# Performance work log

Measured on AMD Instinct MI355X. Metric: run time of the kernel, lower is better.

Reference implementation:

```python
import math
import jax, jax.numpy as jnp
import numpy as np

B, N, NC = 2, 2048, 256
C_S, C_COND, C_Z, C_H, H, PQK, PV = 384, 256, 128, 16, 12, 4, 8
BQ, BK = 32, 128
NBLK = N // BQ
INF, EPS = 1e5, 1e-8
CONCAT = C_Z // 4 + C_H + PV * 4  # per-head output feature dim


def _ln(x, w=None, b=None, eps=1e-5):
    mu = jnp.mean(x, -1, keepdims=True)
    var = jnp.mean((x - mu) ** 2, -1, keepdims=True)
    y = (x - mu) * jax.lax.rsqrt(var + eps)
    if w is not None:
        y = y * w
    if b is not None:
        y = y + b
    return y


def _quat_to_rot(q):
    w, x, y, z = q[..., 0], q[..., 1], q[..., 2], q[..., 3]
    r = jnp.stack([
        1 - 2 * (y * y + z * z), 2 * (x * y - w * z), 2 * (x * z + w * y),
        2 * (x * y + w * z), 1 - 2 * (x * x + z * z), 2 * (y * z - w * x),
        2 * (x * z - w * y), 2 * (y * z + w * x), 1 - 2 * (x * x + y * y),
    ], axis=-1)
    return r.reshape(q.shape[:-1] + (3, 3))


def setup_inputs() -> dict:
    key = jax.random.key(0)
    ks = jax.random.split(key, 24)
    p = lambda k, shp: 0.02 * jax.random.normal(k, shp, dtype=jnp.float32)
    quat = jax.random.normal(ks[5], (B, N, 4), dtype=jnp.float32)
    quat = quat / jnp.linalg.norm(quat, axis=-1, keepdims=True)
    hc = H * C_H
    return {
        "s": jax.random.normal(ks[0], (B, N, C_S), dtype=jnp.float32),
        "cond": jax.random.normal(ks[1], (B, NC, C_COND), dtype=jnp.float32),
        "z": jax.random.normal(ks[2], (B, NBLK, BQ, BK, C_Z), dtype=jnp.float32),
        "trans": jax.random.normal(ks[3], (B, N, 3), dtype=jnp.float32),
        "rots": _quat_to_rot(quat),
        "s_mask": jnp.ones((B, N), dtype=jnp.float32),
        "cond_to_s_idx": jax.random.randint(ks[4], (B, N), 0, NC),
        "ln_cond_w": jnp.ones((C_COND,), dtype=jnp.float32),
        "lin_cond_W": p(ks[6], (C_S, C_COND)),
        "lin_cond_b": jnp.zeros((C_S,), dtype=jnp.float32),
        "lin_cond_nb_W": p(ks[7], (C_S, C_COND)),
        "ln_z_w": jnp.ones((C_Z,), dtype=jnp.float32),
        "ln_z_b": jnp.zeros((C_Z,), dtype=jnp.float32),
        "Wq": p(ks[8], (hc, C_S)),
        "Wk": p(ks[9], (hc, C_S)),
        "Wv": p(ks[10], (hc, C_S)),
        "Wqp": p(ks[11], (H * PQK * 3, C_S)),
        "Wkvp": p(ks[12], (H * (PQK + PV) * 3, C_S)),
        "Wb": p(ks[13], (H, C_Z)),
        "Wdz": p(ks[14], (C_Z // 4, C_Z)),
        "head_weights": jnp.full((H,), 0.541324854612918, dtype=jnp.float32),
        "Wout": p(ks[15], (C_S, H * CONCAT)),
    }


def _forward(s, cond, z, trans, rots, s_mask, cond_to_s_idx,
             ln_cond_w, lin_cond_W, lin_cond_b, lin_cond_nb_W, ln_z_w, ln_z_b,
             Wq, Wk, Wv, Wqp, Wkvp, Wb, Wdz, head_weights, Wout):
    # ---- GatherAdaLN ----
    s_n = _ln(s)
    c_n = _ln(cond, ln_cond_w)
    idx3 = jnp.broadcast_to(cond_to_s_idx[..., None], (B, N, C_S))
    gate = jnp.take_along_axis(c_n @ lin_cond_W.T + lin_cond_b, idx3, axis=1) * s_mask[..., None]
    bias = jnp.take_along_axis(c_n @ lin_cond_nb_W.T, idx3, axis=1) * s_mask[..., None]
    s2 = s_n * jax.nn.sigmoid(gate) + bias
    # ---- pair LN ----
    zn = _ln(z, ln_z_w, ln_z_b)
    # ---- block gather (to_queries / to_keys) ----
    pad = (BK - BQ) // 2
    base = jnp.arange(NBLK)[:, None] * BQ + jnp.arange(BK)[None, :] - pad  # [NBLK, BK]
    validk = (base >= 0) & (base < N)
    kidx = jnp.clip(base, 0, N - 1)

    def to_q(x):
        return x.reshape((B, NBLK, BQ) + x.shape[2:])

    def to_k(x):
        g = x[:, kidx]  # [B, NBLK, BK, ...]
        vm = validk.reshape((1, NBLK, BK) + (1,) * (g.ndim - 3)).astype(g.dtype)
        return g * vm

    q_in, k_in = to_q(s2), to_k(s2)
    q_t, q_R = to_q(trans), to_q(rots)
    k_t = to_k(trans)
    k_R = jnp.where(validk[None, :, :, None, None], rots[:, kidx], jnp.eye(3, dtype=rots.dtype))
    # ---- scalar q/k/v ----
    q = (q_in @ Wq.T).reshape(B, NBLK, BQ, H, C_H)
    k = (k_in @ Wk.T).reshape(B, NBLK, BK, H, C_H)
    v = (k_in @ Wv.T).reshape(B, NBLK, BK, H, C_H)
    # ---- point q/k/v in global frames ----
    qp = (q_in @ Wqp.T).reshape(B, NBLK, BQ, H * PQK, 3)
    q_pts = (jnp.einsum('bnqij,bnqpj->bnqpi', q_R, qp) + q_t[..., None, :]).reshape(B, NBLK, BQ, H, PQK, 3)
    kvp = (k_in @ Wkvp.T).reshape(B, NBLK, BK, H * (PQK + PV), 3)
    kv_pts = (jnp.einsum('bnkij,bnkpj->bnkpi', k_R, kvp) + k_t[..., None, :]).reshape(B, NBLK, BK, H, PQK + PV, 3)
    k_pts, v_pts = kv_pts[..., :PQK, :], kv_pts[..., PQK:, :]
    # ---- logits ----
    b_bias = zn @ Wb.T  # [B,NBLK,BQ,BK,H]
    a = jnp.einsum('bnqhc,bnkhc->bnqkh', q, k) * math.sqrt(1.0 / (3 * C_H)) + b_bias * math.sqrt(1.0 / 3)
    # point bias (cdist form)
    pt = -2.0 * jnp.einsum('bnqhpd,bnkhpd->bnqkh', q_pts, k_pts)
    pt = pt + jnp.sum(q_pts ** 2, axis=(-1, -2))[..., None, :]
    pt = pt + jnp.sum(k_pts ** 2, axis=(-1, -2))[..., None, :, :]
    hw = jax.nn.softplus(head_weights) * math.sqrt(1.0 / (3 * (PQK * 9.0 / 2)))
    pt = pt * hw * (-0.5)
    qm = to_q(s_mask[..., None])  # [B,NBLK,BQ,1]
    km = to_k(s_mask[..., None])  # [B,NBLK,BK,1]
    amask = INF * (qm * jnp.swapaxes(km, -1, -2) - 1.0)  # [B,NBLK,BQ,BK]
    a = a + pt + amask[..., None]
    a = jax.nn.softmax(jnp.swapaxes(a, -1, -2), axis=-1)  # [B,NBLK,BQ,H,BK]
    # ---- outputs ----
    o = jnp.einsum('bnqhk,bnkhc->bnqhc', a, v).reshape(B, NBLK, BQ, H * C_H)
    o_pt = jnp.einsum('bnqhk,bnkhvc->bnqhvc', a, v_pts)
    o_pt = jnp.einsum('bnqij,bnqhvi->bnqhvj', q_R, o_pt - q_t[..., None, None, :])  # R^T (p - t)
    o_pt_norm = jnp.sqrt(jnp.sum(o_pt ** 2, -1) + EPS).reshape(B, NBLK, BQ, H * PV)
    o_pt_flat = o_pt.reshape(B, NBLK, BQ, H * PV * 3)
    pair_z = zn @ Wdz.T  # [B,NBLK,BQ,BK,C_Z//4]
    o_pair = jnp.einsum('bnqhk,bnqkc->bnqhc', a, pair_z).reshape(B, NBLK, BQ, H * (C_Z // 4))
    feats = jnp.concatenate([o, o_pt_flat, o_pt_norm, o_pair], axis=-1)
    return (feats @ Wout.T).reshape(B, N, C_S)


def reference(s, cond, z, trans, rots, s_mask, cond_to_s_idx,
              ln_cond_w, lin_cond_W, lin_cond_b, lin_cond_nb_W, ln_z_w, ln_z_b,
              Wq, Wk, Wv, Wqp, Wkvp, Wb, Wdz, head_weights, Wout):
    return _forward(s, cond, z, trans, rots, s_mask, cond_to_s_idx,
                    ln_cond_w, lin_cond_W, lin_cond_b, lin_cond_nb_W, ln_z_w, ln_z_b,
                    Wq, Wk, Wv, Wqp, Wkvp, Wb, Wdz, head_weights, Wout)
```

## Files before the change

kernel.cpp:

```cpp
#include <hip/hip_runtime.h>
#include <math.h>

constexpr int Bv = 2, Nv = 2048, NCv = 256;
constexpr int CSv = 384, CCONDv = 256;
constexpr int CHv = 16, Hv = 12, PQKv = 4, PVv = 8;
constexpr int BQv = 32, BKv = 128, NBLKv = 64;
constexpr int HC = Hv * CHv;
constexpr int QPD = Hv * PQKv * 3;
constexpr int FEAT = 960;
constexpr int PROJW = 1152;
constexpr float S1 = 0.14433756729740643f;
constexpr float S2 = 0.5773502691896258f;
constexpr float HWS = 0.13608276348795434f;

typedef __attribute__((ext_vector_type(8))) short bf16x8;
typedef __attribute__((ext_vector_type(4))) float f32x4;

__device__ __forceinline__ short f2bf(float f) {
    unsigned u = __float_as_uint(f);
    u += 0x7FFF + ((u >> 16) & 1);
    return (short)(u >> 16);
}
__device__ __forceinline__ float bf2f(short s) {
    return __uint_as_float(((unsigned)(unsigned short)s) << 16);
}
__device__ __forceinline__ unsigned pk2(short lo, short hi) {
    return ((unsigned)(unsigned short)lo) | (((unsigned)(unsigned short)hi) << 16);
}

union BF8 { short s[8]; bf16x8 v; };

__device__ __forceinline__ float blockReduceSum(float v, volatile float* red, int t, int nthr) {
    #pragma unroll
    for (int off = 32; off > 0; off >>= 1) v += __shfl_down(v, off, 64);
    int wid = t >> 6, lane = t & 63, nw = nthr >> 6;
    __syncthreads();
    if (lane == 0) red[wid] = v;
    __syncthreads();
    float r = 0.f;
    for (int w = 0; w < nw; ++w) r += red[w];
    return r;
}

__global__ __launch_bounds__(256) void k_wcvt(const float* __restrict__ Wq,
                                              const float* __restrict__ Wk,
                                              const float* __restrict__ Wv,
                                              const float* __restrict__ Wqp,
                                              const float* __restrict__ Wkvp,
                                              const float* __restrict__ Wg,
                                              const float* __restrict__ Wnb,
                                              short* __restrict__ wsW,
                                              short* __restrict__ wsW2) {
    int i4 = blockIdx.x * 256 + threadIdx.x;
    int off = i4 * 4;
    const float* src;
    short* dst;
    int rel;
    if (off < 442368) {
        dst = wsW; rel = off;
        if (rel < 73728) src = Wq;
        else if (rel < 147456) { src = Wk; rel -= 73728; }
        else if (rel < 221184) { src = Wv; rel -= 147456; }
        else if (rel < 276480) { src = Wqp; rel -= 221184; }
        else { src = Wkvp; rel -= 276480; }
        float4 v = *(const float4*)(src + rel);
        *(uint2*)(dst + off) = make_uint2(pk2(f2bf(v.x), f2bf(v.y)), pk2(f2bf(v.z), f2bf(v.w)));
    } else if (off < 442368 + 196608) {
        int o2 = off - 442368;
        rel = o2;
        if (rel < 98304) src = Wg; else { src = Wnb; rel -= 98304; }
        float4 v = *(const float4*)(src + rel);
        *(uint2*)(wsW2 + o2) = make_uint2(pk2(f2bf(v.x), f2bf(v.y)), pk2(f2bf(v.z), f2bf(v.w)));
    }
}

__global__ __launch_bounds__(256) void k_gemm_bt(const short* __restrict__ A,
                                                 const short* __restrict__ B,
                                                 float* __restrict__ C,
                                                 int K, int ldc) {
    __shared__ short As[128 * 40];
    __shared__ short Bs[128 * 40];
    int t = threadIdx.x;
    int m0 = blockIdx.x * 128, n0 = blockIdx.y * 128;
    int wv = t >> 6, lane = t & 63, lr = lane & 15, quad = lane >> 4;
    int mq = (wv & 1) * 64, nq = (wv >> 1) * 64;
    f32x4 acc[4][4];
    #pragma unroll
    for (int i = 0; i < 4; ++i)
        #pragma unroll
        for (int j = 0; j < 4; ++j) acc[i][j] = 0;

    int r0 = t >> 2, c8 = (t & 3) * 8;
    int r1 = (t + 256) >> 2, c81 = ((t + 256) & 3) * 8;

    for (int k0 = 0; k0 < K; k0 += 32) {
        uint4 a0 = *(const uint4*)(A + (size_t)(m0 + r0) * K + k0 + c8);
        uint4 a1 = *(const uint4*)(A + (size_t)(m0 + r1) * K + k0 + c81);
        uint4 b0 = *(const uint4*)(B + (size_t)(n0 + r0) * K + k0 + c8);
        uint4 b1 = *(const uint4*)(B + (size_t)(n0 + r1) * K + k0 + c81);
        *(uint4*)&As[r0 * 40 + c8] = a0;
        *(uint4*)&As[r1 * 40 + c81] = a1;
        *(uint4*)&Bs[r0 * 40 + c8] = b0;
        *(uint4*)&Bs[r1 * 40 + c81] = b1;
        __syncthreads();
        bf16x8 af[4], bf[4];
        #pragma unroll
        for (int i = 0; i < 4; ++i) {
            af[i] = *(const bf16x8*)&As[(mq + i * 16 + lr) * 40 + quad * 8];
            bf[i] = *(const bf16x8*)&Bs[(nq + i * 16 + lr) * 40 + quad * 8];
        }
        #pragma unroll
        for (int i = 0; i < 4; ++i)
            #pragma unroll
            for (int j = 0; j < 4; ++j)
                acc[i][j] = __builtin_amdgcn_mfma_f32_16x16x32_bf16(af[i], bf[j], acc[i][j], 0, 0, 0);
        __syncthreads();
    }
    #pragma unroll
    for (int i = 0; i < 4; ++i) {
        #pragma unroll
        for (int j = 0; j < 4; ++j) {
            int col = n0 + nq + j * 16 + lr;
            #pragma unroll
            for (int r = 0; r < 4; ++r) {
                int row = m0 + mq + i * 16 + quad * 4 + r;
                C[(size_t)row * ldc + col] = acc[i][j][r];
            }
        }
    }
}

__global__ __launch_bounds__(256) void k_condln(const float* __restrict__ cond,
                                                const float* __restrict__ lnw,
                                                short* __restrict__ cnbf) {
    __shared__ float red[4];
    int row = blockIdx.x;
    int t = threadIdx.x;
    float c = cond[row * CCONDv + t];
    float mu = blockReduceSum(c, red, t, 256) * (1.f / CCONDv);
    float d = c - mu;
    float var = blockReduceSum(d * d, red, t, 256) * (1.f / CCONDv);
    cnbf[row * CCONDv + t] = f2bf(d * rsqrtf(var + 1e-5f) * lnw[t]);
}

__global__ __launch_bounds__(128) void k_s2(const float* __restrict__ s,
                                            const float* __restrict__ gb,
                                            const float* __restrict__ bg,
                                            const int* __restrict__ cidx,
                                            const float* __restrict__ smask,
                                            short* __restrict__ s2bf) {
    __shared__ float red[4];
    int row = blockIdx.x;
    int t = threadIdx.x;
    const float* sr = s + (size_t)row * CSv;
    float x0 = sr[t], x1 = sr[t + 128], x2 = sr[t + 256];
    float mu = blockReduceSum(x0 + x1 + x2, red, t, 128) * (1.f / CSv);
    float d0 = x0 - mu, d1 = x1 - mu, d2 = x2 - mu;
    float var = blockReduceSum(d0 * d0 + d1 * d1 + d2 * d2, red, t, 128) * (1.f / CSv);
    float rs = rsqrtf(var + 1e-5f);
    int b = row / Nv;
    int ci = cidx[row];
    float m = smask[row];
    const float* gbr = gb + (size_t)(b * NCv + ci) * 768;
    float dd[3] = {d0, d1, d2};
    #pragma unroll
    for (int j = 0; j < 3; ++j) {
        int cc = t + j * 128;
        float sn = dd[j] * rs;
        float g = (gbr[cc] + bg[cc]) * m, bi = gbr[384 + cc] * m;
        s2bf[(size_t)row * CSv + cc] = f2bf(sn * (1.f / (1.f + expf(-g))) + bi);
    }
}

__global__ __launch_bounds__(192) void k_post(const float* __restrict__ proj,
                                              const float* __restrict__ rots,
                                              const float* __restrict__ trans,
                                              float* __restrict__ qpts,
                                              float* __restrict__ kpts,
                                              float* __restrict__ vpts,
                                              float* __restrict__ qsq,
                                              float* __restrict__ ksq) {
    __shared__ float R[9], tr[3];
    int row = blockIdx.x;
    int t = threadIdx.x;
    if (t < 9) R[t] = rots[(size_t)row * 9 + t];
    if (t < 3) tr[t] = trans[(size_t)row * 3 + t];
    __syncthreads();
    const float* pr = proj + (size_t)row * PROJW + 576;
    float x = pr[t * 3 + 0], y = pr[t * 3 + 1], z = pr[t * 3 + 2];
    float ox = R[0] * x + R[1] * y + R[2] * z + tr[0];
    float oy = R[3] * x + R[4] * y + R[5] * z + tr[1];
    float oz = R[6] * x + R[7] * y + R[8] * z + tr[2];
    float sq = ox * ox + oy * oy + oz * oz;
    if (t < 48) {
        qpts[(size_t)row * QPD + t * 3 + 0] = ox;
        qpts[(size_t)row * QPD + t * 3 + 1] = oy;
        qpts[(size_t)row * QPD + t * 3 + 2] = oz;
        float s4 = sq + __shfl_xor(sq, 1, 64);
        s4 += __shfl_xor(s4, 2, 64);
        if ((t & 3) == 0) qsq[(size_t)row * Hv + (t >> 2)] = s4;
    } else {
        int p = t - 48;
        int h = p / 12, pp = p % 12;
        if (pp < PQKv) {
            kpts[(size_t)row * QPD + (h * PQKv + pp) * 3 + 0] = ox;
            kpts[(size_t)row * QPD + (h * PQKv + pp) * 3 + 1] = oy;
            kpts[(size_t)row * QPD + (h * PQKv + pp) * 3 + 2] = oz;
            float s4 = sq + __shfl_xor(sq, 1, 64);
            s4 += __shfl_xor(s4, 2, 64);
            if (pp == 0) ksq[(size_t)row * Hv + h] = s4;
        } else {
            int vi = h * PVv + pp - PQKv;
            vpts[(size_t)row * (Hv * PVv * 3) + vi * 3 + 0] = ox;
            vpts[(size_t)row * (Hv * PVv * 3) + vi * 3 + 1] = oy;
            vpts[(size_t)row * (Hv * PVv * 3) + vi * 3 + 2] = oz;
        }
    }
}

__global__ __launch_bounds__(256) void k_prep(const float* __restrict__ Wb,
                                              const float* __restrict__ Wdz,
                                              const float* __restrict__ lnw,
                                              const float* __restrict__ lnb,
                                              short* __restrict__ wp,
                                              float* __restrict__ SB) {
    int t = threadIdx.x;
    if (t < 176) {
        int c = t >> 2, q = t & 3;
        const float* wrow = (c < 12) ? (Wb + (size_t)c * 128) : (Wdz + (size_t)(c - 12) * 128);
        float sacc = 0.f, bacc = 0.f;
        for (int i = q * 32; i < q * 32 + 32; ++i) {
            float wf = wrow[i] * lnw[i];
            short bs = f2bf(wf);
            wp[c * 128 + i] = bs;
            sacc += bf2f(bs);
            bacc += lnb[i] * wrow[i];
        }
        sacc += __shfl_xor(sacc, 1, 64); sacc += __shfl_xor(sacc, 2, 64);
        bacc += __shfl_xor(bacc, 1, 64); bacc += __shfl_xor(bacc, 2, 64);
        if (q == 0) { SB[c] = sacc; SB[48 + c] = bacc; }
    }
    for (int i = t; i < 512; i += 256) wp[44 * 128 + i] = 0;
    if (t >= 176 && t < 180) { SB[t - 132] = 0.f; SB[48 + t - 132] = 0.f; }
}

__global__ __launch_bounds__(256) void k_zproj2(const float* __restrict__ z,
                                                const short* __restrict__ wp,
                                                const float* __restrict__ SB,
                                                float* __restrict__ bbias2,
                                                short* __restrict__ pairzT) {
    __shared__ short zbuf[128 * 136];
    __shared__ short wbuf[48 * 136];
    __shared__ float muL[128], rsL[128], SL[48], BL[48];
    int t = threadIdx.x;
    int bid = blockIdx.x;
    int bblk = bid >> 5, qq = bid & 31;
    size_t row0 = (size_t)bid * 128;

    for (int idx = t; idx < 768; idx += 256) {
        int c = idx >> 4, k8 = idx & 15;
        uint4 v = *(const uint4*)(wp + c * 128 + k8 * 8);
        *(uint4*)&wbuf[c * 136 + k8 * 8] = v;
    }
    if (t < 96) {
        float v = SB[t];
        if (t < 48) SL[t] = v; else BL[t - 48] = v;
    }

    const float4* zsrc = (const float4*)(z + row0 * 128);
    #pragma unroll
    for (int it = 0; it < 16; ++it) {
        int f = it * 256 + t;
        int r = f >> 5, c4 = f & 31;
        float4 v = zsrc[f];
        short s0 = f2bf(v.x), s1 = f2bf(v.y), s2v = f2bf(v.z), s3 = f2bf(v.w);
        *(uint2*)&zbuf[r * 136 + c4 * 4] = make_uint2(pk2(s0, s1), pk2(s2v, s3));
        float sm = v.x + v.y + v.z + v.w;
        float sq = v.x * v.x + v.y * v.y + v.z * v.z + v.w * v.w;
        #pragma unroll
        for (int off = 1; off <= 16; off <<= 1) {
            sm += __shfl_xor(sm, off, 64);
            sq += __shfl_xor(sq, off, 64);
        }
        if ((t & 31) == 0) {
            float mu = sm * (1.f / 128.f);
            float var = sq * (1.f / 128.f) - mu * mu;
            muL[r] = mu;
            rsL[r] = rsqrtf(var + 1e-5f);
        }
    }
    __syncthreads();

    int wv = t >> 6, lane = t & 63;
    int lr = lane & 15, quad = lane >> 4;
    int mb = wv * 32;
    f32x4 acc[2][3];
    #pragma unroll
    for (int i = 0; i < 2; ++i)
        #pragma unroll
        for (int j = 0; j < 3; ++j) acc[i][j] = 0;
    #pragma unroll
    for (int kt = 0; kt < 4; ++kt) {
        int ko = kt * 32 + quad * 8;
        bf16x8 a0 = *(const bf16x8*)&zbuf[(mb + lr) * 136 + ko];
        bf16x8 a1 = *(const bf16x8*)&zbuf[(mb + 16 + lr) * 136 + ko];
        bf16x8 b0 = *(const bf16x8*)&wbuf[lr * 136 + ko];
        bf16x8 b1 = *(const bf16x8*)&wbuf[(16 + lr) * 136 + ko];
        bf16x8 b2 = *(const bf16x8*)&wbuf[(32 + lr) * 136 + ko];
        acc[0][0] = __builtin_amdgcn_mfma_f32_16x16x32_bf16(a0, b0, acc[0][0], 0, 0, 0);
        acc[0][1] = __builtin_amdgcn_mfma_f32_16x16x32_bf16(a0, b1, acc[0][1], 0, 0, 0);
        acc[0][2] = __builtin_amdgcn_mfma_f32_16x16x32_bf16(a0, b2, acc[0][2], 0, 0, 0);
        acc[1][0] = __builtin_amdgcn_mfma_f32_16x16x32_bf16(a1, b0, acc[1][0], 0, 0, 0);
        acc[1][1] = __builtin_amdgcn_mfma_f32_16x16x32_bf16(a1, b1, acc[1][1], 0, 0, 0);
        acc[1][2] = __builtin_amdgcn_mfma_f32_16x16x32_bf16(a1, b2, acc[1][2], 0, 0, 0);
    }

    float* bb_base = bbias2 + (size_t)(bblk * 12) * 4096 + qq * 128;
    short* pz_base = pairzT + (size_t)bid * 32 * 128;
    #pragma unroll
    for (int mt = 0; mt < 2; ++mt) {
        #pragma unroll
        for (int nt = 0; nt < 3; ++nt) {
            int col = nt * 16 + lr;
            int kbase = mb + mt * 16 + quad * 4;
            float ov[4];
            #pragma unroll
            for (int r4 = 0; r4 < 4; ++r4) {
                int rl = kbase + r4;
                ov[r4] = rsL[rl] * (acc[mt][nt][r4] - muL[rl] * SL[col]) + BL[col];
            }
            if (col < 12) {
                *(float4*)&bb_base[(size_t)col * 4096 + kbase] =
                    make_float4(ov[0], ov[1], ov[2], ov[3]);
            } else if (col < 44) {
                int c = col - 12;
                *(uint2*)&pz_base[c * 128 + kbase] =
                    make_uint2(pk2(f2bf(ov[0]), f2bf(ov[1])), pk2(f2bf(ov[2]), f2bf(ov[3])));
            }
        }
    }
}

__global__ __launch_bounds__(512) void k_attn_main(const float* __restrict__ proj,
                                                   const float* __restrict__ qpts,
                                                   const float* __restrict__ kpts,
                                                   const float* __restrict__ vpts,
                                                   const float* __restrict__ qsq,
                                                   const float* __restrict__ ksq,
                                                   const float* __restrict__ bbias2,
                                                   const float* __restrict__ smask,
                                                   const float* __restrict__ head_w,
                                                   short* __restrict__ Aws,
                                                   float* __restrict__ optraw,
                                                   float* __restrict__ feats) {
    __shared__ short kfrag[128 * 40];
    __shared__ short qfrag[32 * 40];
    __shared__ short vtile[128 * 48];
    __shared__ float sc[32 * 132];
    __shared__ short Abuf[32 * 136];
    __shared__ float rowb[32], qmL[32], colb[128], kmL[128];
    __shared__ int   nkgL[128];

    int t = threadIdx.x;
    int hg = blockIdx.x & 1;
    int bblk = blockIdx.x >> 1;
    int b = bblk >> 6, blk = bblk & 63;
    int wv = t >> 6, lane = t & 63;
    int lr = lane & 15, quad = lane >> 4;

    if (t < 128) {
        int nkrel = blk * BQv + t - 48;
        bool valid = (nkrel >= 0) && (nkrel < Nv);
        int nkg = valid ? (b * Nv + nkrel) : -1;
        nkgL[t] = nkg;
        kmL[t] = valid ? smask[nkg] : 0.f;
    }
    __syncthreads();

    for (int hh = 0; hh < 6; ++hh) {
        int h = hg * 6 + hh;
        float hw = log1pf(expf(head_w[h])) * HWS;

        {
            int k = t >> 2, c4 = (t & 3) << 2;
            int g = nkgL[k];
            float4 v = (g >= 0) ? *(const float4*)&proj[(size_t)g * PROJW + 192 + h * 16 + c4]
                                : make_float4(0, 0, 0, 0);
            *(uint2*)&kfrag[k * 40 + c4] =
                make_uint2(pk2(f2bf(v.x), f2bf(v.y)), pk2(f2bf(v.z), f2bf(v.w)));
            kfrag[k * 40 + 28 + (t & 3)] = 0;
        }
        if (t < 384) {
            int k = t / 3, c4 = (t % 3) * 4;
            int g = nkgL[k];
            float4 v = (g >= 0) ? *(const float4*)&kpts[(size_t)g * QPD + h * 12 + c4]
                                : make_float4(0, 0, 0, 0);
            *(uint2*)&kfrag[k * 40 + 16 + c4] =
                make_uint2(pk2(f2bf(v.x), f2bf(v.y)), pk2(f2bf(v.z), f2bf(v.w)));
        }
        if (t < 128) {
            int g = nkgL[t];
            colb[t] = (g >= 0) ? (-0.5f * hw * ksq[(size_t)g * Hv + h]) : 0.f;
            int q = t >> 2, c4 = (t & 3) << 2;
            int nqg = b * Nv + blk * BQv + q;
            float4 v = *(const float4*)&proj[(size_t)nqg * PROJW + h * 16 + c4];
            *(uint2*)&qfrag[q * 40 + c4] =
                make_uint2(pk2(f2bf(S1 * v.x), f2bf(S1 * v.y)),
                           pk2(f2bf(S1 * v.z), f2bf(S1 * v.w)));
            qfrag[q * 40 + 28 + (t & 3)] = 0;
        }
        if (t < 96) {
            int q = t / 3, c4 = (t % 3) * 4;
            int nqg = b * Nv + blk * BQv + q;
            float4 v = *(const float4*)&qpts[(size_t)nqg * QPD + h * 12 + c4];
            *(uint2*)&qfrag[q * 40 + 16 + c4] =
                make_uint2(pk2(f2bf(hw * v.x), f2bf(hw * v.y)),
                           pk2(f2bf(hw * v.z), f2bf(hw * v.w)));
        }
        if (t < 32) {
            int nqg = b * Nv + blk * BQv + t;
            rowb[t] = -0.5f * hw * qsq[(size_t)nqg * Hv + h];
            qmL[t] = smask[nqg];
        }
        for (int i = t; i < 128 * 48; i += 512) {
            int k = i / 48, c = i % 48;
            int g = nkgL[k];
            float v = 0.f;
            if (g >= 0) {
                if (c < 16) v = proj[(size_t)g * PROJW + 384 + h * 16 + c];
                else if (c < 40) v = vpts[(size_t)g * (Hv * PVv * 3) + h * 24 + (c - 16)];
            }
            vtile[k * 48 + c] = f2bf(v);
        }
        __syncthreads();

        f32x4 d[2];
        d[0] = 0; d[1] = 0;
        {
            bf16x8 bfr = *(const bf16x8*)&kfrag[(wv * 16 + lr) * 40 + quad * 8];
            bf16x8 a0 = *(const bf16x8*)&qfrag[lr * 40 + quad * 8];
            bf16x8 a1 = *(const bf16x8*)&qfrag[(16 + lr) * 40 + quad * 8];
            d[0] = __builtin_amdgcn_mfma_f32_16x16x32_bf16(a0, bfr, d[0], 0, 0, 0);
            d[1] = __builtin_amdgcn_mfma_f32_16x16x32_bf16(a1, bfr, d[1], 0, 0, 0);
        }
        {
            const float* bb = bbias2 + (size_t)(bblk * 12 + h) * 4096;
            #pragma unroll
            for (int mt = 0; mt < 2; ++mt) {
                #pragma unroll
                for (int r = 0; r < 4; ++r) {
                    int q = mt * 16 + quad * 4 + r;
                    int k = wv * 16 + lr;
                    float logit = d[mt][r] + rowb[q] + colb[k]
                                + 1e5f * (qmL[q] * kmL[k] - 1.f)
                                + S2 * bb[q * 128 + k];
                    sc[q * 132 + k] = logit;
                }
            }
        }
        __syncthreads();

        {
            int q = t >> 4, i0 = (t & 15) * 8;
            float v[8];
            float m = -3.0e38f;
            #pragma unroll
            for (int j = 0; j < 8; ++j) { v[j] = sc[q * 132 + i0 + j]; m = fmaxf(m, v[j]); }
            #pragma unroll
            for (int off = 1; off <= 8; off <<= 1) m = fmaxf(m, __shfl_xor(m, off, 64));
            float ssum = 0.f;
            #pragma unroll
            for (int j = 0; j < 8; ++j) { v[j] = expf(v[j] - m); ssum += v[j]; }
            #pragma unroll
            for (int off = 1; off <= 8; off <<= 1) ssum += __shfl_xor(ssum, off, 64);
            float inv = 1.f / ssum;
            short a8[8];
            #pragma unroll
            for (int j = 0; j < 8; ++j) a8[j] = f2bf(v[j] * inv);
            uint4 packed = make_uint4(pk2(a8[0], a8[1]), pk2(a8[2], a8[3]),
                                      pk2(a8[4], a8[5]), pk2(a8[6], a8[7]));
            *(uint4*)&Abuf[q * 136 + i0] = packed;
            *(uint4*)&Aws[((size_t)(bblk * 32 + q) * 12 + h) * 128 + i0] = packed;
        }
        __syncthreads();

        if (wv < 6) {
            int mt = wv & 1, nt = wv >> 1;
            f32x4 acc = 0;
            #pragma unroll
            for (int kt = 0; kt < 4; ++kt) {
                bf16x8 a = *(const bf16x8*)&Abuf[(mt * 16 + lr) * 136 + quad * 8 + kt * 32];
                BF8 bb8;
                #pragma unroll
                for (int j = 0; j < 8; ++j)
                    bb8.s[j] = vtile[(kt * 32 + quad * 8 + j) * 48 + nt * 16 + lr];
                acc = __builtin_amdgcn_mfma_f32_16x16x32_bf16(a, bb8.v, acc, 0, 0, 0);
            }
            int c = nt * 16 + lr;
            #pragma unroll
            for (int r = 0; r < 4; ++r) {
                int q = mt * 16 + quad * 4 + r;
                size_t nqg = (size_t)b * Nv + blk * BQv + q;
                if (c < 16) feats[nqg * FEAT + h * 16 + c] = acc[r];
                else if (c < 40) optraw[nqg * 288 + h * 24 + (c - 16)] = acc[r];
            }
        }
        __syncthreads();
    }
}

__global__ __launch_bounds__(64) void k_pair(const short* __restrict__ Aws,
                                             const short* __restrict__ pairzT,
                                             const float* __restrict__ optraw,
                                             const float* __restrict__ rots,
                                             const float* __restrict__ trans,
                                             float* __restrict__ feats) {
    __shared__ unsigned apad_u[16 * 68];
    __shared__ unsigned ppad_u[32 * 68];
    __shared__ float Rt[12];
    int t = threadIdx.x;
    int bid = blockIdx.x;
    int lr = t & 15, quad = t >> 4;

    if (t < 9) Rt[t] = rots[(size_t)bid * 9 + t];
    if (t < 3) Rt[9 + t] = trans[(size_t)bid * 3 + t];

    const unsigned* Asrc = (const unsigned*)(Aws + (size_t)bid * 12 * 128);
    for (int i = t; i < 768; i += 64) {
        int h = i >> 6, w32 = i & 63;
        apad_u[h * 68 + w32] = Asrc[h * 64 + w32];
    }
    for (int i = t; i < 272; i += 64) apad_u[12 * 68 + i] = 0;
    const unsigned* Psrc = (const unsigned*)(pairzT + (size_t)bid * 32 * 128);
    for (int i = t; i < 2048; i += 64) {
        int c = i >> 6, w32 = i & 63;
        ppad_u[c * 68 + w32] = Psrc[c * 64 + w32];
    }
    __syncthreads();

    const short* apad = (const short*)apad_u;
    const short* ppad = (const short*)ppad_u;
    f32x4 acc0 = 0, acc1 = 0;
    #pragma unroll
    for (int kt = 0; kt < 4; ++kt) {
        int ko = quad * 8 + kt * 32;
        bf16x8 a = *(const bf16x8*)&apad[lr * 136 + ko];
        bf16x8 b0 = *(const bf16x8*)&ppad[lr * 136 + ko];
        bf16x8 b1 = *(const bf16x8*)&ppad[(16 + lr) * 136 + ko];
        acc0 = __builtin_amdgcn_mfma_f32_16x16x32_bf16(a, b0, acc0, 0, 0, 0);
        acc1 = __builtin_amdgcn_mfma_f32_16x16x32_bf16(a, b1, acc1, 0, 0, 0);
    }
    float* frow = feats + (size_t)bid * FEAT;
    #pragma unroll
    for (int r = 0; r < 4; ++r) {
        int hh = quad * 4 + r;
        if (hh < 12) {
            frow[576 + hh * 32 + lr] = acc0[r];
            frow[576 + hh * 32 + 16 + lr] = acc1[r];
        }
    }

    for (int p = t; p < 96; p += 64) {
        float x = optraw[(size_t)bid * 288 + p * 3 + 0] - Rt[9];
        float y = optraw[(size_t)bid * 288 + p * 3 + 1] - Rt[10];
        float z = optraw[(size_t)bid * 288 + p * 3 + 2] - Rt[11];
        float lx = Rt[0] * x + Rt[3] * y + Rt[6] * z;
        float ly = Rt[1] * x + Rt[4] * y + Rt[7] * z;
        float lz = Rt[2] * x + Rt[5] * y + Rt[8] * z;
        frow[192 + p * 3 + 0] = lx;
        frow[192 + p * 3 + 1] = ly;
        frow[192 + p * 3 + 2] = lz;
        frow[480 + p] = sqrtf(lx * lx + ly * ly + lz * lz + 1e-8f);
    }
}

__global__ __launch_bounds__(256) void k_out(const float* __restrict__ A,
                                             const float* __restrict__ Wo,
                                             float* __restrict__ C) {
    __shared__ float As[32][65];
    __shared__ float Bs[32][65];
    int t = threadIdx.x;
    int m0 = blockIdx.x * 64;
    int c0 = blockIdx.y * 64;
    int tx = t & 15, ty = t >> 4;
    int lr = t >> 2, lk = (t & 3) * 8;
    float acc[4][4] = {};
    for (int k0 = 0; k0 < FEAT; k0 += 32) {
        const float4* ap = (const float4*)(A + (size_t)(m0 + lr) * FEAT + k0 + lk);
        const float4* bp = (const float4*)(Wo + (size_t)(c0 + lr) * FEAT + k0 + lk);
        float4 a0 = ap[0], a1 = ap[1];
        float4 b0 = bp[0], b1 = bp[1];
        As[lk + 0][lr] = a0.x; As[lk + 1][lr] = a0.y; As[lk + 2][lr] = a0.z; As[lk + 3][lr] = a0.w;
        As[lk + 4][lr] = a1.x; As[lk + 5][lr] = a1.y; As[lk + 6][lr] = a1.z; As[lk + 7][lr] = a1.w;
        Bs[lk + 0][lr] = b0.x; Bs[lk + 1][lr] = b0.y; Bs[lk + 2][lr] = b0.z; Bs[lk + 3][lr] = b0.w;
        Bs[lk + 4][lr] = b1.x; Bs[lk + 5][lr] = b1.y; Bs[lk + 6][lr] = b1.z; Bs[lk + 7][lr] = b1.w;
        __syncthreads();
        #pragma unroll
        for (int kk = 0; kk < 32; ++kk) {
            float a4[4], b4[4];
            #pragma unroll
            for (int i = 0; i < 4; ++i) a4[i] = As[kk][ty * 4 + i];
            #pragma unroll
            for (int j = 0; j < 4; ++j) b4[j] = Bs[kk][tx * 4 + j];
            #pragma unroll
            for (int i = 0; i < 4; ++i)
                #pragma unroll
                for (int j = 0; j < 4; ++j) acc[i][j] += a4[i] * b4[j];
        }
        __syncthreads();
    }
    #pragma unroll
    for (int i = 0; i < 4; ++i)
        #pragma unroll
        for (int j = 0; j < 4; ++j)
            C[(size_t)(m0 + ty * 4 + i) * CSv + c0 + tx * 4 + j] = acc[i][j];
}

extern "C" void kernel_launch(void* const* d_in, const int* in_sizes, int n_in,
                              void* d_out, int out_size, void* d_ws, size_t ws_size,
                              hipStream_t stream) {
    const float* s          = (const float*)d_in[0];
    const float* cond       = (const float*)d_in[1];
    const float* z          = (const float*)d_in[2];
    const float* trans      = (const float*)d_in[3];
    const float* rots       = (const float*)d_in[4];
    const float* smask      = (const float*)d_in[5];
    const int*   cidx       = (const int*)d_in[6];
    const float* ln_cond_w  = (const float*)d_in[7];
    const float* lin_cond_W = (const float*)d_in[8];
    const float* lin_cond_b = (const float*)d_in[9];
    const float* lin_cond_nb_W = (const float*)d_in[10];
    const float* ln_z_w     = (const float*)d_in[11];
    const float* ln_z_b     = (const float*)d_in[12];
    const float* Wq         = (const float*)d_in[13];
    const float* Wk         = (const float*)d_in[14];
    const float* Wv         = (const float*)d_in[15];
    const float* Wqp        = (const float*)d_in[16];
    const float* Wkvp       = (const float*)d_in[17];
    const float* Wb         = (const float*)d_in[18];
    const float* Wdz        = (const float*)d_in[19];
    const float* head_w     = (const float*)d_in[20];
    const float* Wout       = (const float*)d_in[21];
    float* out = (float*)d_out;

    float* p = (float*)d_ws;
    short* wp = (short*)p; p += 3072;
    float* SBp = p; p += 96;
    short* wsW  = (short*)p; p += 221184;
    short* wsW2 = (short*)p; p += 98304;
    short* cnbf = (short*)p; p += 65536;
    float* gb   = p; p += (size_t)512 * 768;
    short* s2bf = (short*)p; p += (size_t)Bv * Nv * CSv / 2;
    float* proj = p; p += (size_t)Bv * Nv * PROJW;
    float* qpts = p; p += (size_t)Bv * Nv * QPD;
    float* kpts = p; p += (size_t)Bv * Nv * QPD;
    float* vpts = p; p += (size_t)Bv * Nv * (Hv * PVv * 3);
    float* qsq  = p; p += (size_t)Bv * Nv * Hv;
    float* ksq  = p; p += (size_t)Bv * Nv * Hv;
    float* bbias2 = p; p += (size_t)128 * 12 * 4096;
    short* pairzT = (short*)p; p += (size_t)128 * 32 * 32 * 64;
    short* Aws    = (short*)p; p += (size_t)4096 * 12 * 64;
    float* optraw = p; p += (size_t)4096 * 288;
    float* feats  = p; p += (size_t)Bv * Nv * FEAT;

    k_wcvt<<<624, 256, 0, stream>>>(Wq, Wk, Wv, Wqp, Wkvp, lin_cond_W, lin_cond_nb_W,
                                    wsW, wsW2);
    k_prep<<<1, 256, 0, stream>>>(Wb, Wdz, ln_z_w, ln_z_b, wp, SBp);
    k_condln<<<Bv * NCv, 256, 0, stream>>>(cond, ln_cond_w, cnbf);
    k_gemm_bt<<<dim3(4, 6), 256, 0, stream>>>(cnbf, wsW2, gb, CCONDv, 768);
    k_s2<<<Bv * Nv, 128, 0, stream>>>(s, gb, lin_cond_b, cidx, smask, s2bf);
    k_gemm_bt<<<dim3(32, 9), 256, 0, stream>>>(s2bf, wsW, proj, CSv, PROJW);
    k_post<<<Bv * Nv, 192, 0, stream>>>(proj, rots, trans, qpts, kpts, vpts, qsq, ksq);
    k_zproj2<<<Bv * NBLKv * BQv, 256, 0, stream>>>(z, wp, SBp, bbias2, pairzT);
    k_attn_main<<<Bv * NBLKv * 2, 512, 0, stream>>>(proj, qpts, kpts, vpts, qsq, ksq,
                                                    bbias2, smask, head_w, Aws, optraw, feats);
    k_pair<<<Bv * NBLKv * BQv, 64, 0, stream>>>(Aws, pairzT, optraw, rots, trans, feats);
    k_out<<<dim3(64, 6), 256, 0, stream>>>(feats, Wout, out);
}
```

Before: 650.6 us.

## Split attention across six head-pair blocks, store pair bias in bf16, transpose V tile

The attention kernel now launches six blocks per query block, each handling two heads instead of six, to raise parallelism and occupancy (launch bounds set to 6). The pair bias is pre-scaled and stored as bf16, halving its write and read traffic. V is staged transposed in shared memory so MFMA B-operands load as single vector reads, and V loads use float4. The pair kernel reads A and pair_z directly from global instead of staging them through LDS, and softmax uses fast exp. This costs extra redundant per-block setup, and bf16 bias adds rounding error.

```diff
diff --git a/kernel.cpp b/kernel.cpp
--- a/kernel.cpp
+++ b/kernel.cpp
@@ -27,8 +27,6 @@
 __device__ __forceinline__ unsigned pk2(short lo, short hi) {
     return ((unsigned)(unsigned short)lo) | (((unsigned)(unsigned short)hi) << 16);
 }
-
-union BF8 { short s[8]; bf16x8 v; };
 
 __device__ __forceinline__ float blockReduceSum(float v, volatile float* red, int t, int nthr) {
     #pragma unroll
@@ -247,7 +245,7 @@
 __global__ __launch_bounds__(256) void k_zproj2(const float* __restrict__ z,
                                                 const short* __restrict__ wp,
                                                 const float* __restrict__ SB,
-                                                float* __restrict__ bbias2,
+                                                short* __restrict__ bbias2,
                                                 short* __restrict__ pairzT) {
     __shared__ short zbuf[128 * 136];
     __shared__ short wbuf[48 * 136];
@@ -315,7 +313,7 @@
         acc[1][2] = __builtin_amdgcn_mfma_f32_16x16x32_bf16(a1, b2, acc[1][2], 0, 0, 0);
     }
 
-    float* bb_base = bbias2 + (size_t)(bblk * 12) * 4096 + qq * 128;
+    short* bb_base = bbias2 + (size_t)(bblk * 12) * 4096 + qq * 128;
     short* pz_base = pairzT + (size_t)bid * 32 * 128;
     #pragma unroll
     for (int mt = 0; mt < 2; ++mt) {
@@ -330,8 +328,9 @@
                 ov[r4] = rsL[rl] * (acc[mt][nt][r4] - muL[rl] * SL[col]) + BL[col];
             }
             if (col < 12) {
-                *(float4*)&bb_base[(size_t)col * 4096 + kbase] =
-                    make_float4(ov[0], ov[1], ov[2], ov[3]);
+                *(uint2*)&bb_base[(size_t)col * 4096 + kbase] =
+                    make_uint2(pk2(f2bf(S2 * ov[0]), f2bf(S2 * ov[1])),
+                               pk2(f2bf(S2 * ov[2]), f2bf(S2 * ov[3])));
             } else if (col < 44) {
                 int c = col - 12;
                 *(uint2*)&pz_base[c * 128 + kbase] =
@@ -341,29 +340,29 @@
     }
 }
 
-__global__ __launch_bounds__(512) void k_attn_main(const float* __restrict__ proj,
-                                                   const float* __restrict__ qpts,
-                                                   const float* __restrict__ kpts,
-                                                   const float* __restrict__ vpts,
-                                                   const float* __restrict__ qsq,
-                                                   const float* __restrict__ ksq,
-                                                   const float* __restrict__ bbias2,
-                                                   const float* __restrict__ smask,
-                                                   const float* __restrict__ head_w,
-                                                   short* __restrict__ Aws,
-                                                   float* __restrict__ optraw,
-                                                   float* __restrict__ feats) {
+__global__ __launch_bounds__(512, 6) void k_attn_main(const float* __restrict__ proj,
+                                                      const float* __restrict__ qpts,
+                                                      const float* __restrict__ kpts,
+                                                      const float* __restrict__ vpts,
+                                                      const float* __restrict__ qsq,
+                                                      const float* __restrict__ ksq,
+                                                      const short* __restrict__ bbias2,
+                                                      const float* __restrict__ smask,
+                                                      const float* __restrict__ head_w,
+                                                      short* __restrict__ Aws,
+                                                      float* __restrict__ optraw,
+                                                      float* __restrict__ feats) {
     __shared__ short kfrag[128 * 40];
     __shared__ short qfrag[32 * 40];
-    __shared__ short vtile[128 * 48];
+    __shared__ short vtileT[48 * 136];
     __shared__ float sc[32 * 132];
     __shared__ short Abuf[32 * 136];
     __shared__ float rowb[32], qmL[32], colb[128], kmL[128];
     __shared__ int   nkgL[128];
 
     int t = threadIdx.x;
-    int hg = blockIdx.x & 1;
-    int bblk = blockIdx.x >> 1;
+    int hp = blockIdx.x % 6;
+    int bblk = blockIdx.x / 6;
     int b = bblk >> 6, blk = bblk & 63;
     int wv = t >> 6, lane = t & 63;
     int lr = lane & 15, quad = lane >> 4;
@@ -375,10 +374,14 @@
         nkgL[t] = nkg;
         kmL[t] = valid ? smask[nkg] : 0.f;
     }
+    {
+        int c = 40 + (t >> 6), k2 = (t & 63) * 2;
+        *(unsigned*)&vtileT[c * 136 + k2] = 0;
+    }
     __syncthreads();
 
-    for (int hh = 0; hh < 6; ++hh) {
-        int h = hg * 6 + hh;
+    for (int hh = 0; hh < 2; ++hh) {
+        int h = hp * 2 + hh;
         float hw = log1pf(expf(head_w[h])) * HWS;
 
         {
@@ -419,18 +422,30 @@
         }
         if (t < 32) {
             int nqg = b * Nv + blk * BQv + t;
+            rowb[t] = -0.5f * hw * qsq[(size_t)nqg * Hv + t >= 0 ? (size_t)nqg * Hv + h - ((size_t)nqg * Hv + h) + (size_t)nqg * Hv + h : 0];
             rowb[t] = -0.5f * hw * qsq[(size_t)nqg * Hv + h];
             qmL[t] = smask[nqg];
         }
-        for (int i = t; i < 128 * 48; i += 512) {
-            int k = i / 48, c = i % 48;
+        {
+            int k = t >> 2, c0 = (t & 3) << 2;
             int g = nkgL[k];
-            float v = 0.f;
-            if (g >= 0) {
-                if (c < 16) v = proj[(size_t)g * PROJW + 384 + h * 16 + c];
-                else if (c < 40) v = vpts[(size_t)g * (Hv * PVv * 3) + h * 24 + (c - 16)];
-            }
-            vtile[k * 48 + c] = f2bf(v);
+            float4 v = (g >= 0) ? *(const float4*)&proj[(size_t)g * PROJW + 384 + h * 16 + c0]
+                                : make_float4(0, 0, 0, 0);
+            vtileT[(c0 + 0) * 136 + k] = f2bf(v.x);
+            vtileT[(c0 + 1) * 136 + k] = f2bf(v.y);
+            vtileT[(c0 + 2) * 136 + k] = f2bf(v.z);
+            vtileT[(c0 + 3) * 136 + k] = f2bf(v.w);
+        }
+        for (int i = t; i < 768; i += 512) {
+            int k = i / 6, p = i % 6;
+            int g = nkgL[k];
+            float4 v = (g >= 0) ? *(const float4*)&vpts[(size_t)g * (Hv * PVv * 3) + h * 24 + p * 4]
+                                : make_float4(0, 0, 0, 0);
+            int c0 = 16 + p * 4;
+            vtileT[(c0 + 0) * 136 + k] = f2bf(v.x);
+            vtileT[(c0 + 1) * 136 + k] = f2bf(v.y);
+            vtileT[(c0 + 2) * 136 + k] = f2bf(v.z);
+            vtileT[(c0 + 3) * 136 + k] = f2bf(v.w);
         }
         __syncthreads();
 
@@ -444,7 +459,7 @@
             d[1] = __builtin_amdgcn_mfma_f32_16x16x32_bf16(a1, bfr, d[1], 0, 0, 0);
         }
         {
-            const float* bb = bbias2 + (size_t)(bblk * 12 + h) * 4096;
+            const short* bb = bbias2 + (size_t)(bblk * 12 + h) * 4096;
             #pragma unroll
             for (int mt = 0; mt < 2; ++mt) {
                 #pragma unroll
@@ -453,7 +468,7 @@
                     int k = wv * 16 + lr;
                     float logit = d[mt][r] + rowb[q] + colb[k]
                                 + 1e5f * (qmL[q] * kmL[k] - 1.f)
-                                + S2 * bb[q * 128 + k];
+                                + bf2f(bb[q * 128 + k]);
                     sc[q * 132 + k] = logit;
                 }
             }
@@ -470,7 +485,7 @@
             for (int off = 1; off <= 8; off <<= 1) m = fmaxf(m, __shfl_xor(m, off, 64));
             float ssum = 0.f;
             #pragma unroll
-            for (int j = 0; j < 8; ++j) { v[j] = expf(v[j] - m); ssum += v[j]; }
+            for (int j = 0; j < 8; ++j) { v[j] = __expf(v[j] - m); ssum += v[j]; }
             #pragma unroll
             for (int off = 1; off <= 8; off <<= 1) ssum += __shfl_xor(ssum, off, 64);
             float inv = 1.f / ssum;
@@ -490,11 +505,8 @@
             #pragma unroll
             for (int kt = 0; kt < 4; ++kt) {
                 bf16x8 a = *(const bf16x8*)&Abuf[(mt * 16 + lr) * 136 + quad * 8 + kt * 32];
-                BF8 bb8;
-                #pragma unroll
-                for (int j = 0; j < 8; ++j)
-                    bb8.s[j] = vtile[(kt * 32 + quad * 8 + j) * 48 + nt * 16 + lr];
-                acc = __builtin_amdgcn_mfma_f32_16x16x32_bf16(a, bb8.v, acc, 0, 0, 0);
+                bf16x8 bv = *(const bf16x8*)&vtileT[(nt * 16 + lr) * 136 + quad * 8 + kt * 32];
+                acc = __builtin_amdgcn_mfma_f32_16x16x32_bf16(a, bv, acc, 0, 0, 0);
             }
             int c = nt * 16 + lr;
             #pragma unroll
@@ -515,8 +527,6 @@
                                              const float* __restrict__ rots,
                                              const float* __restrict__ trans,
                                              float* __restrict__ feats) {
-    __shared__ unsigned apad_u[16 * 68];
-    __shared__ unsigned ppad_u[32 * 68];
     __shared__ float Rt[12];
     int t = threadIdx.x;
     int bid = blockIdx.x;
@@ -524,29 +534,18 @@
 
     if (t < 9) Rt[t] = rots[(size_t)bid * 9 + t];
     if (t < 3) Rt[9 + t] = trans[(size_t)bid * 3 + t];
-
-    const unsigned* Asrc = (const unsigned*)(Aws + (size_t)bid * 12 * 128);
-    for (int i = t; i < 768; i += 64) {
-        int h = i >> 6, w32 = i & 63;
-        apad_u[h * 68 + w32] = Asrc[h * 64 + w32];
-    }
-    for (int i = t; i < 272; i += 64) apad_u[12 * 68 + i] = 0;
-    const unsigned* Psrc = (const unsigned*)(pairzT + (size_t)bid * 32 * 128);
-    for (int i = t; i < 2048; i += 64) {
-        int c = i >> 6, w32 = i & 63;
-        ppad_u[c * 68 + w32] = Psrc[c * 64 + w32];
-    }
     __syncthreads();
 
-    const short* apad = (const short*)apad_u;
-    const short* ppad = (const short*)ppad_u;
+    const short* Ab = Aws + (size_t)bid * 1536;
+    const short* Pb = pairzT + (size_t)bid * 4096;
     f32x4 acc0 = 0, acc1 = 0;
     #pragma unroll
     for (int kt = 0; kt < 4; ++kt) {
-        int ko = quad * 8 + kt * 32;
-        bf16x8 a = *(const bf16x8*)&apad[lr * 136 + ko];
-        bf16x8 b0 = *(const bf16x8*)&ppad[lr * 136 + ko];
-        bf16x8 b1 = *(const bf16x8*)&ppad[(16 + lr) * 136 + ko];
+        int ko = kt * 32 + quad * 8;
+        bf16x8 a = 0;
+        if (lr < 12) a = *(const bf16x8*)&Ab[lr * 128 + ko];
+        bf16x8 b0 = *(const bf16x8*)&Pb[lr * 128 + ko];
+        bf16x8 b1 = *(const bf16x8*)&Pb[(16 + lr) * 128 + ko];
         acc0 = __builtin_amdgcn_mfma_f32_16x16x32_bf16(a, b0, acc0, 0, 0, 0);
         acc1 = __builtin_amdgcn_mfma_f32_16x16x32_bf16(a, b1, acc1, 0, 0, 0);
     }
@@ -657,7 +656,7 @@
     float* vpts = p; p += (size_t)Bv * Nv * (Hv * PVv * 3);
     float* qsq  = p; p += (size_t)Bv * Nv * Hv;
     float* ksq  = p; p += (size_t)Bv * Nv * Hv;
-    float* bbias2 = p; p += (size_t)128 * 12 * 4096;
+    short* bbias2 = (short*)p; p += (size_t)128 * 12 * 4096 / 2;
     short* pairzT = (short*)p; p += (size_t)128 * 32 * 32 * 64;
     short* Aws    = (short*)p; p += (size_t)4096 * 12 * 64;
     float* optraw = p; p += (size_t)4096 * 288;
@@ -672,7 +671,7 @@
     k_gemm_bt<<<dim3(32, 9), 256, 0, stream>>>(s2bf, wsW, proj, CSv, PROJW);
     k_post<<<Bv * Nv, 192, 0, stream>>>(proj, rots, trans, qpts, kpts, vpts, qsq, ksq);
     k_zproj2<<<Bv * NBLKv * BQv, 256, 0, stream>>>(z, wp, SBp, bbias2, pairzT);
-    k_attn_main<<<Bv * NBLKv * 2, 512, 0, stream>>>(proj, qpts, kpts, vpts, qsq, ksq,
+    k_attn_main<<<Bv * NBLKv * 6, 512, 0, stream>>>(proj, qpts, kpts, vpts, qsq, ksq,
                                                     bbias2, smask, head_w, Aws, optraw, feats);
     k_pair<<<Bv * NBLKv * BQv, 64, 0, stream>>>(Aws, pairzT, optraw, rots, trans, feats);
     k_out<<<dim3(64, 6), 256, 0, stream>>>(feats, Wout, out);
```

Result: faster. 616.8 us (-5.2%).
